# Optimization experiments

Measured on AMD Instinct MI355X. Metric: run time of the kernel, lower is better.

Reference implementation:

```python
import jax, jax.numpy as jnp
import numpy as np

N = 100000      # nodes
E = 1600000     # edges (avg degree 16)
DIN = 48        # input features
H = 48          # hidden
DOUT = 16       # output classes


def setup_inputs() -> dict:
    key = jax.random.key(0)
    ks = jax.random.split(key, 20)
    inp = {
        "x": jax.random.normal(ks[0], (N, DIN), jnp.float32),
        "edge_index": jax.random.randint(ks[1], (2, E), 0, N, jnp.int32),
    }
    # (name, in_dim, out_dim) for the 2-layer MLP in each of 3 GINConvs + final fc
    layers = [("11", DIN, H), ("12", H, H),
              ("21", H, H), ("22", H, H),
              ("31", H, H), ("32", H, H),
              ("f1", H, H), ("f2", H, DOUT)]
    for i, (nm, din, dout) in enumerate(layers):
        inp["w" + nm] = jax.random.normal(ks[2 + i], (din, dout), jnp.float32) / np.float32(np.sqrt(din))
        inp["b" + nm] = jax.random.normal(ks[10 + i], (dout,), jnp.float32) * 0.01
    return inp


def reference(x, edge_index, w11, b11, w12, b12, w21, b21, w22, b22,
              w31, b31, w32, b32, wf1, bf1, wf2, bf2):
    src, dst = edge_index[0], edge_index[1]
    n = x.shape[0]

    def gin_conv(h, w1, b1, w2, b2):
        # scatter-sum neighbor aggregation: sum_{j in N(i)} h_j
        agg = jax.ops.segment_sum(h[src], dst, num_segments=n)  # [N, d]
        h2 = h + agg  # eps = 0 (PyG GINConv default): (1+eps)*x + agg
        h2 = jax.nn.relu(h2 @ w1 + b1)
        return jax.nn.relu(h2 @ w2 + b2)

    h = gin_conv(x, w11, b11, w12, b12)
    h = gin_conv(h, w21, b21, w22, b22)
    h = gin_conv(h, w31, b31, w32, b32)
    # final fc head: Linear -> ReLU -> Linear
    return jax.nn.relu(h @ wf1 + bf1) @ wf2 + bf2
```

## Files before the change

### kernel.cpp

```cpp
#include <hip/hip_runtime.h>

#define NN 100000
#define NE 1600000
#define D 48
#define BK_SHIFT 8
#define BK_NODES 256
#define NBK 391
#define CAP 5120
#define EPB 4096
#define NBINB 391
#define ST 72

typedef _Float16 f16x8 __attribute__((ext_vector_type(8)));
typedef float f32x4 __attribute__((ext_vector_type(4)));


__global__ __launch_bounds__(256) void prepbin(
    const int* __restrict__ src, const int* __restrict__ dst,
    int* __restrict__ bucketLen, int* __restrict__ arena,
    const float* __restrict__ x,
    const float* __restrict__ w11, const float* __restrict__ w12,
    const float* __restrict__ w21, const float* __restrict__ w22,
    const float* __restrict__ w31, const float* __restrict__ w32,
    const float* __restrict__ wf1, const float* __restrict__ wf2,
    _Float16* __restrict__ wp, uint4* __restrict__ outh) {
    __shared__ int sCnt[NBK];
    __shared__ int sBase[NBK];
    int b = blockIdx.x;
    int tid = threadIdx.x;
    if (b < NBINB) {
        for (int i = tid; i < NBK; i += 256) sCnt[i] = 0;
        __syncthreads();
        int e0 = b * EPB;
        int eend = e0 + EPB;
        if (eend > NE) eend = NE;
        for (int i = e0 + tid; i < eend; i += 256) atomicAdd(&sCnt[dst[i] >> BK_SHIFT], 1);
        __syncthreads();
        for (int i = tid; i < NBK; i += 256) sBase[i] = atomicAdd(&bucketLen[i], sCnt[i]);
        __syncthreads();
        for (int i = tid; i < NBK; i += 256) sCnt[i] = 0;
        __syncthreads();
        for (int i = e0 + tid; i < eend; i += 256) {
            int d = dst[i];
            int bk = d >> BK_SHIFT;
            int off = atomicAdd(&sCnt[bk], 1) + sBase[bk];
            if (off < CAP) arena[bk * CAP + off] = ((d & (BK_NODES - 1)) << 17) | src[i];
        }
    } else if (b < NBINB + 8) {
        int l = b - NBINB;
        const float* W;
        int NL = 48;
        switch (l) {
            case 0: W = w11; break;
            case 1: W = w12; break;
            case 2: W = w21; break;
            case 3: W = w22; break;
            case 4: W = w31; break;
            case 5: W = w32; break;
            case 6: W = wf1; break;
            default: W = wf2; NL = 16; break;
        }
        _Float16* T = wp + l * 3072;
        int total = 64 * NL;
        for (int i = tid; i < total; i += 256) {
            int j = i & 7;
            int m = i >> 3;
            int g = m / NL;
            int nn = m - g * NL;
            int k = g * 8 + j;
            T[i] = (k < 48) ? (_Float16)W[k * NL + nn] : (_Float16)0.f;
        }
    } else {
        int i = (b - NBINB - 8) * 256 + tid;
        if (i < NN * 6) {
            const float4* p = (const float4*)(x + (size_t)i * 8);
            float4 a = p[0], bb = p[1];
            union { _Float16 h[8]; uint4 u; } pk;
            pk.h[0] = (_Float16)a.x; pk.h[1] = (_Float16)a.y;
            pk.h[2] = (_Float16)a.z; pk.h[3] = (_Float16)a.w;
            pk.h[4] = (_Float16)bb.x; pk.h[5] = (_Float16)bb.y;
            pk.h[6] = (_Float16)bb.z; pk.h[7] = (_Float16)bb.w;
            outh[i] = pk.u;
        }
    }
}


__global__ __launch_bounds__(256) void csr_from_bins(
    const int* __restrict__ arena, const int* __restrict__ bucketLen,
    int* __restrict__ rowptr, int* __restrict__ colidx) {
    __shared__ int sCnt[BK_NODES];
    __shared__ int sTot[256];
    int b = blockIdx.x;
    int tid = threadIdx.x;
    int len = bucketLen[b];
    if (len > CAP) len = CAP;
    const int* ar = arena + (size_t)b * CAP;
    int colBase = b * CAP;
    int nodeBase = b << BK_SHIFT;

    sCnt[tid] = 0;
    __syncthreads();
    for (int i = tid; i < len; i += 256) atomicAdd(&sCnt[ar[i] >> 17], 1);
    __syncthreads();

    int mine = sCnt[tid];
    sTot[tid] = mine;
    __syncthreads();
    for (int off = 1; off < 256; off <<= 1) {
        int add = 0;
        if (tid >= off) add = sTot[tid - off];
        __syncthreads();
        if (tid >= off) sTot[tid] += add;
        __syncthreads();
    }
    int excl = sTot[tid] - mine;
    int node = nodeBase + tid;
    if (node < NN) rowptr[node] = colBase + excl;
    __syncthreads();
    sCnt[tid] = colBase + excl;
    __syncthreads();
    for (int i = tid; i < len; i += 256) {
        int p = ar[i];
        int pos = atomicAdd(&sCnt[p >> 17], 1);
        colidx[pos] = p & 0x1FFFF;
    }
}


__device__ __forceinline__ void mfma_layer48(
    const _Float16* __restrict__ wp, const float* __restrict__ bias,
    const _Float16* src, _Float16* dst, int lane) {
    int am = lane & 15, q = lane >> 4;
    f16x8 a0 = *(const f16x8*)(src + am * ST + q * 8);
    f16x8 a1 = *(const f16x8*)(src + am * ST + 32 + q * 8);
#pragma unroll
    for (int t = 0; t < 3; ++t) {
        f16x8 b0 = *(const f16x8*)(wp + ((q) * 48 + t * 16 + am) * 8);
        f16x8 b1 = *(const f16x8*)(wp + ((4 + q) * 48 + t * 16 + am) * 8);
        float bv = bias[t * 16 + am];
        f32x4 c = {bv, bv, bv, bv};
        c = __builtin_amdgcn_mfma_f32_16x16x32_f16(a0, b0, c, 0, 0, 0);
        c = __builtin_amdgcn_mfma_f32_16x16x32_f16(a1, b1, c, 0, 0, 0);
#pragma unroll
        for (int r = 0; r < 4; ++r) {
            float v = fmaxf(c[r], 0.f);
            dst[(q * 4 + r) * ST + t * 16 + am] = (_Float16)v;
        }
    }
}


__device__ __forceinline__ void gather_stage(const uint4* __restrict__ hin4,
                                             const int* __restrict__ rowptr,
                                             const int* __restrict__ col,
                                             int bend,
                                             _Float16* s0, _Float16* s1,
                                             int base, int wv, int lane, int n) {
    for (int i = lane; i < 16 * 3; i += 64) {
        int r = i / 3, cq = i % 3;
        *(uint4*)(s0 + r * ST + 48 + cq * 8) = make_uint4(0u, 0u, 0u, 0u);
        *(uint4*)(s1 + r * ST + 48 + cq * 8) = make_uint4(0u, 0u, 0u, 0u);
    }
    int s = lane & 7;
    int c = lane >> 3;
    bool act = (c < 6);
    int cc = act ? c : 0;
    int nb = base + wv * 16;
    for (int nl = 0; nl < 16; nl += 2) {
        int node0 = nb + nl;
        int node1 = node0 + 1;
        f16x8 acc0 = {0, 0, 0, 0, 0, 0, 0, 0};
        f16x8 acc1 = {0, 0, 0, 0, 0, 0, 0, 0};
        int e00 = 0, e01 = 0, e10 = 0, e11 = 0;
        if (node0 < n) {
            e00 = rowptr[node0];
            e01 = rowptr[node0 + 1];
        }
        if (node1 < n) {
            e10 = e01;
            e11 = ((node1 & (BK_NODES - 1)) == BK_NODES - 1 || node1 == n - 1)
                      ? bend : rowptr[node1 + 1];
        }
        if (act) {
            int ebA = e00, ebB = e10;
            while (ebA < e01 || ebB < e11) {
                int eA0 = ebA + s, eA1 = ebA + 8 + s;
                int eB0 = ebB + s, eB1 = ebB + 8 + s;
                bool okA0 = eA0 < e01, okA1 = eA1 < e01;
                bool okB0 = eB0 < e11, okB1 = eB1 < e11;
                int iA0 = col[okA0 ? eA0 : e00] & 0x1FFFF;
                int iA1 = col[okA1 ? eA1 : e00] & 0x1FFFF;
                int iB0 = col[okB0 ? eB0 : e10] & 0x1FFFF;
                int iB1 = col[okB1 ? eB1 : e10] & 0x1FFFF;
                uint4 vA0 = hin4[(size_t)iA0 * 6 + cc];
                uint4 vA1 = hin4[(size_t)iA1 * 6 + cc];
                uint4 vB0 = hin4[(size_t)iB0 * 6 + cc];
                uint4 vB1 = hin4[(size_t)iB1 * 6 + cc];
                if (!okA0) vA0 = make_uint4(0u, 0u, 0u, 0u);
                if (!okA1) vA1 = make_uint4(0u, 0u, 0u, 0u);
                if (!okB0) vB0 = make_uint4(0u, 0u, 0u, 0u);
                if (!okB1) vB1 = make_uint4(0u, 0u, 0u, 0u);
                acc0 += *(const f16x8*)&vA0;
                acc0 += *(const f16x8*)&vA1;
                acc1 += *(const f16x8*)&vB0;
                acc1 += *(const f16x8*)&vB1;
                ebA += 16;
                ebB += 16;
            }
        }
        union { f16x8 f; int i[4]; } a0, a1, bx;
        a0.f = acc0;
        a1.f = acc1;
#pragma unroll
        for (int m = 1; m <= 4; m <<= 1) {
            bx.i[0] = __shfl_xor(a0.i[0], m);
            bx.i[1] = __shfl_xor(a0.i[1], m);
            bx.i[2] = __shfl_xor(a0.i[2], m);
            bx.i[3] = __shfl_xor(a0.i[3], m);
            a0.f += bx.f;
            bx.i[0] = __shfl_xor(a1.i[0], m);
            bx.i[1] = __shfl_xor(a1.i[1], m);
            bx.i[2] = __shfl_xor(a1.i[2], m);
            bx.i[3] = __shfl_xor(a1.i[3], m);
            a1.f += bx.f;
        }
        if (s == 0 && act) {
            union { f16x8 f; uint4 u; } r0, r1;
            r0.f = (f16x8){0, 0, 0, 0, 0, 0, 0, 0};
            r1.f = (f16x8){0, 0, 0, 0, 0, 0, 0, 0};
            if (node0 < n) {
                uint4 self = hin4[(size_t)node0 * 6 + c];
                r0.f = a0.f + *(const f16x8*)&self;
            }
            if (node1 < n) {
                uint4 self = hin4[(size_t)node1 * 6 + c];
                r1.f = a1.f + *(const f16x8*)&self;
            }
            *(uint4*)(s0 + nl * ST + c * 8) = r0.u;
            *(uint4*)(s0 + (nl + 1) * ST + c * 8) = r1.u;
        }
    }
    __builtin_amdgcn_wave_barrier();
}

__global__ __launch_bounds__(256) void conv_fused(
    const uint4* __restrict__ hin4, const int* __restrict__ rowptr,
    const int* __restrict__ col, const int* __restrict__ bucketLen,
    const _Float16* __restrict__ wp1, const float* __restrict__ B1,
    const _Float16* __restrict__ wp2, const float* __restrict__ B2,
    _Float16* __restrict__ hout, int n) {
    __shared__ __align__(16) _Float16 HA[2 * 64 * ST];
    int tid = threadIdx.x;
    int base = blockIdx.x * 64;
    int lane = tid & 63;
    int wv = tid >> 6;
    _Float16* s0 = HA + wv * 16 * ST;
    _Float16* s1 = HA + 64 * ST + wv * 16 * ST;

    int bucket = base >> BK_SHIFT;
    int blen = bucketLen[bucket];
    if (blen > CAP) blen = CAP;
    int bend = bucket * CAP + blen;

    gather_stage(hin4, rowptr, col, bend, s0, s1, base, wv, lane, n);
    mfma_layer48(wp1, B1, s0, s1, lane);
    __builtin_amdgcn_wave_barrier();

    int am = lane & 15, q = lane >> 4;
    f16x8 a0 = *(const f16x8*)(s1 + am * ST + q * 8);
    f16x8 a1 = *(const f16x8*)(s1 + am * ST + 32 + q * 8);
    int g0 = base + wv * 16;
#pragma unroll
    for (int t = 0; t < 3; ++t) {
        f16x8 b0 = *(const f16x8*)(wp2 + ((q) * 48 + t * 16 + am) * 8);
        f16x8 b1 = *(const f16x8*)(wp2 + ((4 + q) * 48 + t * 16 + am) * 8);
        float bv = B2[t * 16 + am];
        f32x4 c = {bv, bv, bv, bv};
        c = __builtin_amdgcn_mfma_f32_16x16x32_f16(a0, b0, c, 0, 0, 0);
        c = __builtin_amdgcn_mfma_f32_16x16x32_f16(a1, b1, c, 0, 0, 0);
#pragma unroll
        for (int r = 0; r < 4; ++r) {
            int node = g0 + q * 4 + r;
            if (node < n) {
                float v = fmaxf(c[r], 0.f);
                hout[(size_t)node * D + t * 16 + am] = (_Float16)v;
            }
        }
    }
}

__global__ __launch_bounds__(256) void tail_fused(
    const uint4* __restrict__ hin4, const int* __restrict__ rowptr,
    const int* __restrict__ col, const int* __restrict__ bucketLen,
    const _Float16* __restrict__ wp1, const float* __restrict__ B1,
    const _Float16* __restrict__ wp2, const float* __restrict__ B2,
    const _Float16* __restrict__ wp3, const float* __restrict__ B3,
    const _Float16* __restrict__ wp4, const float* __restrict__ B4,
    float* __restrict__ out, int n) {
    __shared__ __align__(16) _Float16 HA[2 * 64 * ST];
    int tid = threadIdx.x;
    int base = blockIdx.x * 64;
    int lane = tid & 63;
    int wv = tid >> 6;
    _Float16* s0 = HA + wv * 16 * ST;
    _Float16* s1 = HA + 64 * ST + wv * 16 * ST;

    int bucket = base >> BK_SHIFT;
    int blen = bucketLen[bucket];
    if (blen > CAP) blen = CAP;
    int bend = bucket * CAP + blen;

    gather_stage(hin4, rowptr, col, bend, s0, s1, base, wv, lane, n);
    mfma_layer48(wp1, B1, s0, s1, lane);
    __builtin_amdgcn_wave_barrier();
    mfma_layer48(wp2, B2, s1, s0, lane);
    __builtin_amdgcn_wave_barrier();
    mfma_layer48(wp3, B3, s0, s1, lane);
    __builtin_amdgcn_wave_barrier();

    int am = lane & 15, q = lane >> 4;
    f16x8 a0 = *(const f16x8*)(s1 + am * ST + q * 8);
    f16x8 a1 = *(const f16x8*)(s1 + am * ST + 32 + q * 8);
    f16x8 b0 = *(const f16x8*)(wp4 + ((q) * 16 + am) * 8);
    f16x8 b1 = *(const f16x8*)(wp4 + ((4 + q) * 16 + am) * 8);
    float bv = B4[am];
    f32x4 c = {bv, bv, bv, bv};
    c = __builtin_amdgcn_mfma_f32_16x16x32_f16(a0, b0, c, 0, 0, 0);
    c = __builtin_amdgcn_mfma_f32_16x16x32_f16(a1, b1, c, 0, 0, 0);
    int g0 = base + wv * 16;
#pragma unroll
    for (int r = 0; r < 4; ++r) {
        int node = g0 + q * 4 + r;
        if (node < n) out[(size_t)node * 16 + am] = c[r];
    }
}


extern "C" void kernel_launch(void* const* d_in, const int* in_sizes, int n_in,
                              void* d_out, int out_size, void* d_ws, size_t ws_size,
                              hipStream_t stream) {
    const int n = NN, e = NE;
    const float* x = (const float*)d_in[0];
    const int* ei = (const int*)d_in[1];
    const int* src = ei;
    const int* dst = ei + e;
    const float* w11 = (const float*)d_in[2];
    const float* b11 = (const float*)d_in[3];
    const float* w12 = (const float*)d_in[4];
    const float* b12 = (const float*)d_in[5];
    const float* w21 = (const float*)d_in[6];
    const float* b21 = (const float*)d_in[7];
    const float* w22 = (const float*)d_in[8];
    const float* b22 = (const float*)d_in[9];
    const float* w31 = (const float*)d_in[10];
    const float* b31 = (const float*)d_in[11];
    const float* w32 = (const float*)d_in[12];
    const float* b32 = (const float*)d_in[13];
    const float* wf1 = (const float*)d_in[14];
    const float* bf1 = (const float*)d_in[15];
    const float* wf2 = (const float*)d_in[16];
    const float* bf2 = (const float*)d_in[17];
    float* out = (float*)d_out;

    uint4* HAa = (uint4*)d_ws;
    uint4* HAb = HAa + (size_t)n * 6;
    _Float16* WP = (_Float16*)(HAb + (size_t)n * 6);
    int* rowptr = (int*)(WP + 8 * 3072);
    int* colidx = rowptr + (n + 1);
    int* arena = colidx + (size_t)NBK * CAP;
    int* bucketLen = arena + (size_t)NBK * CAP;
    size_t needed = (size_t)((char*)(bucketLen + NBK) - (char*)d_ws);
    if (needed > ws_size) return;

    const _Float16* wp11 = WP + 0 * 3072;
    const _Float16* wp12 = WP + 1 * 3072;
    const _Float16* wp21 = WP + 2 * 3072;
    const _Float16* wp22 = WP + 3 * 3072;
    const _Float16* wp31 = WP + 4 * 3072;
    const _Float16* wp32 = WP + 5 * 3072;
    const _Float16* wpf1 = WP + 6 * 3072;
    const _Float16* wpf2 = WP + 7 * 3072;

    hipMemsetAsync(bucketLen, 0, NBK * sizeof(int), stream);
    int gPB = NBINB + 8 + (n * 6 + 255) / 256;
    prepbin<<<gPB, 256, 0, stream>>>(src, dst, bucketLen, arena, x,
                                     w11, w12, w21, w22, w31, w32, wf1, wf2,
                                     WP, HAa);
    csr_from_bins<<<NBK, 256, 0, stream>>>(arena, bucketLen, rowptr, colidx);

    int gConv = (n + 63) / 64;

    conv_fused<<<gConv, 256, 0, stream>>>(HAa, rowptr, colidx, bucketLen,
                                          wp11, b11, wp12, b12, (_Float16*)HAb, n);
    conv_fused<<<gConv, 256, 0, stream>>>(HAb, rowptr, colidx, bucketLen,
                                          wp21, b21, wp22, b22, (_Float16*)HAa, n);
    tail_fused<<<gConv, 256, 0, stream>>>(HAa, rowptr, colidx, bucketLen,
                                          wp31, b31, wp32, b32,
                                          wpf1, bf1, wpf2, bf2, out, n);
}
```

Measured before the change: 273.5 us.

## Replace bucketed CSR build with fixed-capacity per-node adjacency slots

Drops the two-pass bucket binning and the csr_from_bins kernel. Each edge is now written directly into a fixed 64-slot row for its destination node using a global per-node atomic counter, and the gather reads those padded rows. This removes a kernel launch and the prefix-scan pass, at the cost of 1.6M global atomics on a 100K-entry counter array and a much larger padded arena. Any node with in-degree above 64 silently loses edges. Nontemporal loads and stores are also added for the column indices and the outputs.

```diff
diff --git a/kernel.cpp b/kernel.cpp
--- a/kernel.cpp
+++ b/kernel.cpp
@@ -3,12 +3,9 @@
 #define NN 100000
 #define NE 1600000
 #define D 48
-#define BK_SHIFT 8
-#define BK_NODES 256
-#define NBK 391
-#define CAP 5120
+#define CAPN 64
 #define EPB 4096
-#define NBINB 391
+#define NBB 391
 #define ST 72
 
 typedef _Float16 f16x8 __attribute__((ext_vector_type(8)));
@@ -17,37 +14,26 @@
 
 __global__ __launch_bounds__(256) void prepbin(
     const int* __restrict__ src, const int* __restrict__ dst,
-    int* __restrict__ bucketLen, int* __restrict__ arena,
+    int* __restrict__ cnt, int* __restrict__ arena,
     const float* __restrict__ x,
     const float* __restrict__ w11, const float* __restrict__ w12,
     const float* __restrict__ w21, const float* __restrict__ w22,
     const float* __restrict__ w31, const float* __restrict__ w32,
     const float* __restrict__ wf1, const float* __restrict__ wf2,
     _Float16* __restrict__ wp, uint4* __restrict__ outh) {
-    __shared__ int sCnt[NBK];
-    __shared__ int sBase[NBK];
     int b = blockIdx.x;
     int tid = threadIdx.x;
-    if (b < NBINB) {
-        for (int i = tid; i < NBK; i += 256) sCnt[i] = 0;
-        __syncthreads();
+    if (b < NBB) {
         int e0 = b * EPB;
         int eend = e0 + EPB;
         if (eend > NE) eend = NE;
-        for (int i = e0 + tid; i < eend; i += 256) atomicAdd(&sCnt[dst[i] >> BK_SHIFT], 1);
-        __syncthreads();
-        for (int i = tid; i < NBK; i += 256) sBase[i] = atomicAdd(&bucketLen[i], sCnt[i]);
-        __syncthreads();
-        for (int i = tid; i < NBK; i += 256) sCnt[i] = 0;
-        __syncthreads();
         for (int i = e0 + tid; i < eend; i += 256) {
             int d = dst[i];
-            int bk = d >> BK_SHIFT;
-            int off = atomicAdd(&sCnt[bk], 1) + sBase[bk];
-            if (off < CAP) arena[bk * CAP + off] = ((d & (BK_NODES - 1)) << 17) | src[i];
-        }
-    } else if (b < NBINB + 8) {
-        int l = b - NBINB;
+            int off = atomicAdd(&cnt[d], 1);
+            if (off < CAPN) arena[(size_t)d * CAPN + off] = src[i];
+        }
+    } else if (b < NBB + 8) {
+        int l = b - NBB;
         const float* W;
         int NL = 48;
         switch (l) {
@@ -71,7 +57,7 @@
             T[i] = (k < 48) ? (_Float16)W[k * NL + nn] : (_Float16)0.f;
         }
     } else {
-        int i = (b - NBINB - 8) * 256 + tid;
+        int i = (b - NBB - 8) * 256 + tid;
         if (i < NN * 6) {
             const float4* p = (const float4*)(x + (size_t)i * 8);
             float4 a = p[0], bb = p[1];
@@ -86,48 +72,6 @@
 }
 
 
-__global__ __launch_bounds__(256) void csr_from_bins(
-    const int* __restrict__ arena, const int* __restrict__ bucketLen,
-    int* __restrict__ rowptr, int* __restrict__ colidx) {
-    __shared__ int sCnt[BK_NODES];
-    __shared__ int sTot[256];
-    int b = blockIdx.x;
-    int tid = threadIdx.x;
-    int len = bucketLen[b];
-    if (len > CAP) len = CAP;
-    const int* ar = arena + (size_t)b * CAP;
-    int colBase = b * CAP;
-    int nodeBase = b << BK_SHIFT;
-
-    sCnt[tid] = 0;
-    __syncthreads();
-    for (int i = tid; i < len; i += 256) atomicAdd(&sCnt[ar[i] >> 17], 1);
-    __syncthreads();
-
-    int mine = sCnt[tid];
-    sTot[tid] = mine;
-    __syncthreads();
-    for (int off = 1; off < 256; off <<= 1) {
-        int add = 0;
-        if (tid >= off) add = sTot[tid - off];
-        __syncthreads();
-        if (tid >= off) sTot[tid] += add;
-        __syncthreads();
-    }
-    int excl = sTot[tid] - mine;
-    int node = nodeBase + tid;
-    if (node < NN) rowptr[node] = colBase + excl;
-    __syncthreads();
-    sCnt[tid] = colBase + excl;
-    __syncthreads();
-    for (int i = tid; i < len; i += 256) {
-        int p = ar[i];
-        int pos = atomicAdd(&sCnt[p >> 17], 1);
-        colidx[pos] = p & 0x1FFFF;
-    }
-}
-
-
 __device__ __forceinline__ void mfma_layer48(
     const _Float16* __restrict__ wp, const float* __restrict__ bias,
     const _Float16* src, _Float16* dst, int lane) {
@@ -152,9 +96,8 @@
 
 
 __device__ __forceinline__ void gather_stage(const uint4* __restrict__ hin4,
-                                             const int* __restrict__ rowptr,
+                                             const int* __restrict__ cnt,
                                              const int* __restrict__ col,
-                                             int bend,
                                              _Float16* s0, _Float16* s1,
                                              int base, int wv, int lane, int n) {
     for (int i = lane; i < 16 * 3; i += 64) {
@@ -170,29 +113,23 @@
     for (int nl = 0; nl < 16; nl += 2) {
         int node0 = nb + nl;
         int node1 = node0 + 1;
+        int len0 = 0, len1 = 0;
+        if (node0 < n) { len0 = cnt[node0]; if (len0 > CAPN) len0 = CAPN; }
+        if (node1 < n) { len1 = cnt[node1]; if (len1 > CAPN) len1 = CAPN; }
+        const int* colA = col + (size_t)(node0 < n ? node0 : 0) * CAPN;
+        const int* colB = col + (size_t)(node1 < n ? node1 : 0) * CAPN;
         f16x8 acc0 = {0, 0, 0, 0, 0, 0, 0, 0};
         f16x8 acc1 = {0, 0, 0, 0, 0, 0, 0, 0};
-        int e00 = 0, e01 = 0, e10 = 0, e11 = 0;
-        if (node0 < n) {
-            e00 = rowptr[node0];
-            e01 = rowptr[node0 + 1];
-        }
-        if (node1 < n) {
-            e10 = e01;
-            e11 = ((node1 & (BK_NODES - 1)) == BK_NODES - 1 || node1 == n - 1)
-                      ? bend : rowptr[node1 + 1];
-        }
+        int lmax = len0 > len1 ? len0 : len1;
         if (act) {
-            int ebA = e00, ebB = e10;
-            while (ebA < e01 || ebB < e11) {
-                int eA0 = ebA + s, eA1 = ebA + 8 + s;
-                int eB0 = ebB + s, eB1 = ebB + 8 + s;
-                bool okA0 = eA0 < e01, okA1 = eA1 < e01;
-                bool okB0 = eB0 < e11, okB1 = eB1 < e11;
-                int iA0 = col[okA0 ? eA0 : e00] & 0x1FFFF;
-                int iA1 = col[okA1 ? eA1 : e00] & 0x1FFFF;
-                int iB0 = col[okB0 ? eB0 : e10] & 0x1FFFF;
-                int iB1 = col[okB1 ? eB1 : e10] & 0x1FFFF;
+            for (int k = 0; k < lmax; k += 16) {
+                int k0 = k + s, k1 = k + 8 + s;
+                bool okA0 = k0 < len0, okA1 = k1 < len0;
+                bool okB0 = k0 < len1, okB1 = k1 < len1;
+                int iA0 = __builtin_nontemporal_load(colA + (okA0 ? k0 : 0)) & 0x1FFFF;
+                int iA1 = __builtin_nontemporal_load(colA + (okA1 ? k1 : 0)) & 0x1FFFF;
+                int iB0 = __builtin_nontemporal_load(colB + (okB0 ? k0 : 0)) & 0x1FFFF;
+                int iB1 = __builtin_nontemporal_load(colB + (okB1 ? k1 : 0)) & 0x1FFFF;
                 uint4 vA0 = hin4[(size_t)iA0 * 6 + cc];
                 uint4 vA1 = hin4[(size_t)iA1 * 6 + cc];
                 uint4 vB0 = hin4[(size_t)iB0 * 6 + cc];
@@ -205,8 +142,6 @@
                 acc0 += *(const f16x8*)&vA1;
                 acc1 += *(const f16x8*)&vB0;
                 acc1 += *(const f16x8*)&vB1;
-                ebA += 16;
-                ebB += 16;
             }
         }
         union { f16x8 f; int i[4]; } a0, a1, bx;
@@ -245,8 +180,8 @@
 }
 
 __global__ __launch_bounds__(256) void conv_fused(
-    const uint4* __restrict__ hin4, const int* __restrict__ rowptr,
-    const int* __restrict__ col, const int* __restrict__ bucketLen,
+    const uint4* __restrict__ hin4, const int* __restrict__ cnt,
+    const int* __restrict__ col,
     const _Float16* __restrict__ wp1, const float* __restrict__ B1,
     const _Float16* __restrict__ wp2, const float* __restrict__ B2,
     _Float16* __restrict__ hout, int n) {
@@ -258,12 +193,7 @@
     _Float16* s0 = HA + wv * 16 * ST;
     _Float16* s1 = HA + 64 * ST + wv * 16 * ST;
 
-    int bucket = base >> BK_SHIFT;
-    int blen = bucketLen[bucket];
-    if (blen > CAP) blen = CAP;
-    int bend = bucket * CAP + blen;
-
-    gather_stage(hin4, rowptr, col, bend, s0, s1, base, wv, lane, n);
+    gather_stage(hin4, cnt, col, s0, s1, base, wv, lane, n);
     mfma_layer48(wp1, B1, s0, s1, lane);
     __builtin_amdgcn_wave_barrier();
 
@@ -284,15 +214,16 @@
             int node = g0 + q * 4 + r;
             if (node < n) {
                 float v = fmaxf(c[r], 0.f);
-                hout[(size_t)node * D + t * 16 + am] = (_Float16)v;
+                __builtin_nontemporal_store((_Float16)v,
+                                            &hout[(size_t)node * D + t * 16 + am]);
             }
         }
     }
 }
 
 __global__ __launch_bounds__(256) void tail_fused(
-    const uint4* __restrict__ hin4, const int* __restrict__ rowptr,
-    const int* __restrict__ col, const int* __restrict__ bucketLen,
+    const uint4* __restrict__ hin4, const int* __restrict__ cnt,
+    const int* __restrict__ col,
     const _Float16* __restrict__ wp1, const float* __restrict__ B1,
     const _Float16* __restrict__ wp2, const float* __restrict__ B2,
     const _Float16* __restrict__ wp3, const float* __restrict__ B3,
@@ -306,12 +237,7 @@
     _Float16* s0 = HA + wv * 16 * ST;
     _Float16* s1 = HA + 64 * ST + wv * 16 * ST;
 
-    int bucket = base >> BK_SHIFT;
-    int blen = bucketLen[bucket];
-    if (blen > CAP) blen = CAP;
-    int bend = bucket * CAP + blen;
-
-    gather_stage(hin4, rowptr, col, bend, s0, s1, base, wv, lane, n);
+    gather_stage(hin4, cnt, col, s0, s1, base, wv, lane, n);
     mfma_layer48(wp1, B1, s0, s1, lane);
     __builtin_amdgcn_wave_barrier();
     mfma_layer48(wp2, B2, s1, s0, lane);
@@ -332,7 +258,7 @@
 #pragma unroll
     for (int r = 0; r < 4; ++r) {
         int node = g0 + q * 4 + r;
-        if (node < n) out[(size_t)node * 16 + am] = c[r];
+        if (node < n) __builtin_nontemporal_store(c[r], &out[(size_t)node * 16 + am]);
     }
 }
 
@@ -366,11 +292,9 @@
     uint4* HAa = (uint4*)d_ws;
     uint4* HAb = HAa + (size_t)n * 6;
     _Float16* WP = (_Float16*)(HAb + (size_t)n * 6);
-    int* rowptr = (int*)(WP + 8 * 3072);
-    int* colidx = rowptr + (n + 1);
-    int* arena = colidx + (size_t)NBK * CAP;
-    int* bucketLen = arena + (size_t)NBK * CAP;
-    size_t needed = (size_t)((char*)(bucketLen + NBK) - (char*)d_ws);
+    int* cnt = (int*)(WP + 8 * 3072);
+    int* arena = cnt + n;
+    size_t needed = (size_t)((char*)(arena + (size_t)n * CAPN) - (char*)d_ws);
     if (needed > ws_size) return;
 
     const _Float16* wp11 = WP + 0 * 3072;
@@ -382,20 +306,19 @@
     const _Float16* wpf1 = WP + 6 * 3072;
     const _Float16* wpf2 = WP + 7 * 3072;
 
-    hipMemsetAsync(bucketLen, 0, NBK * sizeof(int), stream);
-    int gPB = NBINB + 8 + (n * 6 + 255) / 256;
-    prepbin<<<gPB, 256, 0, stream>>>(src, dst, bucketLen, arena, x,
+    hipMemsetAsync(cnt, 0, (size_t)n * sizeof(int), stream);
+    int gPB = NBB + 8 + (n * 6 + 255) / 256;
+    prepbin<<<gPB, 256, 0, stream>>>(src, dst, cnt, arena, x,
                                      w11, w12, w21, w22, w31, w32, wf1, wf2,
                                      WP, HAa);
-    csr_from_bins<<<NBK, 256, 0, stream>>>(arena, bucketLen, rowptr, colidx);
 
     int gConv = (n + 63) / 64;
 
-    conv_fused<<<gConv, 256, 0, stream>>>(HAa, rowptr, colidx, bucketLen,
+    conv_fused<<<gConv, 256, 0, stream>>>(HAa, cnt, arena,
                                           wp11, b11, wp12, b12, (_Float16*)HAb, n);
-    conv_fused<<<gConv, 256, 0, stream>>>(HAb, rowptr, colidx, bucketLen,
+    conv_fused<<<gConv, 256, 0, stream>>>(HAb, cnt, arena,
                                           wp21, b21, wp22, b22, (_Float16*)HAa, n);
-    tail_fused<<<gConv, 256, 0, stream>>>(HAa, rowptr, colidx, bucketLen,
+    tail_fused<<<gConv, 256, 0, stream>>>(HAa, cnt, arena,
                                           wp31, b31, wp32, b32,
                                           wpf1, bf1, wpf2, bf2, out, n);
 }
```

New measurement: 368.4 us. 34.7% more time.

## Split CSR build into 64-node groups and rotate bucket atomic order

Applied to the files above, without the earlier changes.

The CSR construction kernel now runs one block per 64-node group (four groups per 256-node bin) instead of one block per bin. Each group block rescans its parent bin and keeps only its quarter, using a wave shuffle scan in place of a shared-memory scan with many barriers. Each group writes its own end offset for the conv kernels to use. The binning kernel also rotates the order of its global bucket atomics per block and skips zero counts, to reduce contention on the same counters. The trade-off is that every bin slice is read four times, and the per-group capacity adds a new truncation point if a group has too many edges.

```diff
diff --git a/kernel.cpp b/kernel.cpp
--- a/kernel.cpp
+++ b/kernel.cpp
@@ -9,6 +9,8 @@
 #define CAP 5120
 #define EPB 4096
 #define NBINB 391
+#define NG 1563
+#define CAPG 1344
 #define ST 72
 
 typedef _Float16 f16x8 __attribute__((ext_vector_type(8)));
@@ -36,7 +38,13 @@
         if (eend > NE) eend = NE;
         for (int i = e0 + tid; i < eend; i += 256) atomicAdd(&sCnt[dst[i] >> BK_SHIFT], 1);
         __syncthreads();
-        for (int i = tid; i < NBK; i += 256) sBase[i] = atomicAdd(&bucketLen[i], sCnt[i]);
+        int rot = (b * 101) % NBK;
+        for (int k = tid; k < NBK; k += 256) {
+            int i = k + rot;
+            if (i >= NBK) i -= NBK;
+            int v = sCnt[i];
+            sBase[i] = v ? atomicAdd(&bucketLen[i], v) : 0;
+        }
         __syncthreads();
         for (int i = tid; i < NBK; i += 256) sCnt[i] = 0;
         __syncthreads();
@@ -44,7 +52,7 @@
             int d = dst[i];
             int bk = d >> BK_SHIFT;
             int off = atomicAdd(&sCnt[bk], 1) + sBase[bk];
-            if (off < CAP) arena[bk * CAP + off] = ((d & (BK_NODES - 1)) << 17) | src[i];
+            if (off < CAP) arena[(size_t)bk * CAP + off] = ((d & (BK_NODES - 1)) << 17) | src[i];
         }
     } else if (b < NBINB + 8) {
         int l = b - NBINB;
@@ -86,44 +94,53 @@
 }
 
 
-__global__ __launch_bounds__(256) void csr_from_bins(
+__global__ __launch_bounds__(256) void csr64(
     const int* __restrict__ arena, const int* __restrict__ bucketLen,
-    int* __restrict__ rowptr, int* __restrict__ colidx) {
-    __shared__ int sCnt[BK_NODES];
-    __shared__ int sTot[256];
-    int b = blockIdx.x;
+    int* __restrict__ rowptr, int* __restrict__ gEnd, int* __restrict__ colidx) {
+    __shared__ int sCnt[64];
+    __shared__ int sPos[64];
+    int g = blockIdx.x;
     int tid = threadIdx.x;
-    int len = bucketLen[b];
-    if (len > CAP) len = CAP;
-    const int* ar = arena + (size_t)b * CAP;
-    int colBase = b * CAP;
-    int nodeBase = b << BK_SHIFT;
-
-    sCnt[tid] = 0;
+    int parent = g >> 2;
+    int quarter = g & 3;
+    int plen = bucketLen[parent];
+    if (plen > CAP) plen = CAP;
+    const int* slice = arena + (size_t)parent * CAP;
+    int gBase = g * CAPG;
+
+    if (tid < 64) sCnt[tid] = 0;
     __syncthreads();
-    for (int i = tid; i < len; i += 256) atomicAdd(&sCnt[ar[i] >> 17], 1);
+    for (int i = tid; i < plen; i += 256) {
+        int p = slice[i];
+        if ((p >> 23) == quarter) atomicAdd(&sCnt[(p >> 17) & 63], 1);
+    }
     __syncthreads();
-
-    int mine = sCnt[tid];
-    sTot[tid] = mine;
+    if (tid < 64) {
+        int v = sCnt[tid];
+        int xx = v;
+#pragma unroll
+        for (int off = 1; off < 64; off <<= 1) {
+            int y = __shfl_up(xx, off);
+            if (tid >= off) xx += y;
+        }
+        int excl = xx - v;
+        if (excl > CAPG) excl = CAPG;
+        int node = (g << 6) + tid;
+        if (node < NN) rowptr[node] = gBase + excl;
+        sPos[tid] = gBase + excl;
+        if (tid == 63) {
+            int tot = xx > CAPG ? CAPG : xx;
+            gEnd[g] = gBase + tot;
+        }
+    }
     __syncthreads();
-    for (int off = 1; off < 256; off <<= 1) {
-        int add = 0;
-        if (tid >= off) add = sTot[tid - off];
-        __syncthreads();
-        if (tid >= off) sTot[tid] += add;
-        __syncthreads();
-    }
-    int excl = sTot[tid] - mine;
-    int node = nodeBase + tid;
-    if (node < NN) rowptr[node] = colBase + excl;
-    __syncthreads();
-    sCnt[tid] = colBase + excl;
-    __syncthreads();
-    for (int i = tid; i < len; i += 256) {
-        int p = ar[i];
-        int pos = atomicAdd(&sCnt[p >> 17], 1);
-        colidx[pos] = p & 0x1FFFF;
+    int lim = gBase + CAPG;
+    for (int i = tid; i < plen; i += 256) {
+        int p = slice[i];
+        if ((p >> 23) == quarter) {
+            int slot = atomicAdd(&sPos[(p >> 17) & 63], 1);
+            if (slot < lim) colidx[slot] = p & 0x1FFFF;
+        }
     }
 }
 
@@ -154,7 +171,7 @@
 __device__ __forceinline__ void gather_stage(const uint4* __restrict__ hin4,
                                              const int* __restrict__ rowptr,
                                              const int* __restrict__ col,
-                                             int bend,
+                                             int gend,
                                              _Float16* s0, _Float16* s1,
                                              int base, int wv, int lane, int n) {
     for (int i = lane; i < 16 * 3; i += 64) {
@@ -170,6 +187,7 @@
     for (int nl = 0; nl < 16; nl += 2) {
         int node0 = nb + nl;
         int node1 = node0 + 1;
+        int r1 = wv * 16 + nl + 1;
         f16x8 acc0 = {0, 0, 0, 0, 0, 0, 0, 0};
         f16x8 acc1 = {0, 0, 0, 0, 0, 0, 0, 0};
         int e00 = 0, e01 = 0, e10 = 0, e11 = 0;
@@ -179,8 +197,7 @@
         }
         if (node1 < n) {
             e10 = e01;
-            e11 = ((node1 & (BK_NODES - 1)) == BK_NODES - 1 || node1 == n - 1)
-                      ? bend : rowptr[node1 + 1];
+            e11 = (r1 == 63 || node1 == n - 1) ? gend : rowptr[node1 + 1];
         }
         if (act) {
             int ebA = e00, ebB = e10;
@@ -226,19 +243,19 @@
             a1.f += bx.f;
         }
         if (s == 0 && act) {
-            union { f16x8 f; uint4 u; } r0, r1;
-            r0.f = (f16x8){0, 0, 0, 0, 0, 0, 0, 0};
-            r1.f = (f16x8){0, 0, 0, 0, 0, 0, 0, 0};
+            union { f16x8 f; uint4 u; } r0u, r1u;
+            r0u.f = (f16x8){0, 0, 0, 0, 0, 0, 0, 0};
+            r1u.f = (f16x8){0, 0, 0, 0, 0, 0, 0, 0};
             if (node0 < n) {
                 uint4 self = hin4[(size_t)node0 * 6 + c];
-                r0.f = a0.f + *(const f16x8*)&self;
+                r0u.f = a0.f + *(const f16x8*)&self;
             }
             if (node1 < n) {
                 uint4 self = hin4[(size_t)node1 * 6 + c];
-                r1.f = a1.f + *(const f16x8*)&self;
+                r1u.f = a1.f + *(const f16x8*)&self;
             }
-            *(uint4*)(s0 + nl * ST + c * 8) = r0.u;
-            *(uint4*)(s0 + (nl + 1) * ST + c * 8) = r1.u;
+            *(uint4*)(s0 + nl * ST + c * 8) = r0u.u;
+            *(uint4*)(s0 + (nl + 1) * ST + c * 8) = r1u.u;
         }
     }
     __builtin_amdgcn_wave_barrier();
@@ -246,24 +263,22 @@
 
 __global__ __launch_bounds__(256) void conv_fused(
     const uint4* __restrict__ hin4, const int* __restrict__ rowptr,
-    const int* __restrict__ col, const int* __restrict__ bucketLen,
+    const int* __restrict__ col, const int* __restrict__ gEnd,
     const _Float16* __restrict__ wp1, const float* __restrict__ B1,
     const _Float16* __restrict__ wp2, const float* __restrict__ B2,
     _Float16* __restrict__ hout, int n) {
     __shared__ __align__(16) _Float16 HA[2 * 64 * ST];
     int tid = threadIdx.x;
-    int base = blockIdx.x * 64;
+    int g = blockIdx.x;
+    int base = g << 6;
     int lane = tid & 63;
     int wv = tid >> 6;
     _Float16* s0 = HA + wv * 16 * ST;
     _Float16* s1 = HA + 64 * ST + wv * 16 * ST;
 
-    int bucket = base >> BK_SHIFT;
-    int blen = bucketLen[bucket];
-    if (blen > CAP) blen = CAP;
-    int bend = bucket * CAP + blen;
-
-    gather_stage(hin4, rowptr, col, bend, s0, s1, base, wv, lane, n);
+    int gend = gEnd[g];
+
+    gather_stage(hin4, rowptr, col, gend, s0, s1, base, wv, lane, n);
     mfma_layer48(wp1, B1, s0, s1, lane);
     __builtin_amdgcn_wave_barrier();
 
@@ -292,7 +307,7 @@
 
 __global__ __launch_bounds__(256) void tail_fused(
     const uint4* __restrict__ hin4, const int* __restrict__ rowptr,
-    const int* __restrict__ col, const int* __restrict__ bucketLen,
+    const int* __restrict__ col, const int* __restrict__ gEnd,
     const _Float16* __restrict__ wp1, const float* __restrict__ B1,
     const _Float16* __restrict__ wp2, const float* __restrict__ B2,
     const _Float16* __restrict__ wp3, const float* __restrict__ B3,
@@ -300,18 +315,16 @@
     float* __restrict__ out, int n) {
     __shared__ __align__(16) _Float16 HA[2 * 64 * ST];
     int tid = threadIdx.x;
-    int base = blockIdx.x * 64;
+    int g = blockIdx.x;
+    int base = g << 6;
     int lane = tid & 63;
     int wv = tid >> 6;
     _Float16* s0 = HA + wv * 16 * ST;
     _Float16* s1 = HA + 64 * ST + wv * 16 * ST;
 
-    int bucket = base >> BK_SHIFT;
-    int blen = bucketLen[bucket];
-    if (blen > CAP) blen = CAP;
-    int bend = bucket * CAP + blen;
-
-    gather_stage(hin4, rowptr, col, bend, s0, s1, base, wv, lane, n);
+    int gend = gEnd[g];
+
+    gather_stage(hin4, rowptr, col, gend, s0, s1, base, wv, lane, n);
     mfma_layer48(wp1, B1, s0, s1, lane);
     __builtin_amdgcn_wave_barrier();
     mfma_layer48(wp2, B2, s1, s0, lane);
@@ -367,8 +380,9 @@
     uint4* HAb = HAa + (size_t)n * 6;
     _Float16* WP = (_Float16*)(HAb + (size_t)n * 6);
     int* rowptr = (int*)(WP + 8 * 3072);
-    int* colidx = rowptr + (n + 1);
-    int* arena = colidx + (size_t)NBK * CAP;
+    int* gEnd = rowptr + n;
+    int* colidx = gEnd + NG;
+    int* arena = colidx + (size_t)NG * CAPG;
     int* bucketLen = arena + (size_t)NBK * CAP;
     size_t needed = (size_t)((char*)(bucketLen + NBK) - (char*)d_ws);
     if (needed > ws_size) return;
@@ -387,15 +401,15 @@
     prepbin<<<gPB, 256, 0, stream>>>(src, dst, bucketLen, arena, x,
                                      w11, w12, w21, w22, w31, w32, wf1, wf2,
                                      WP, HAa);
-    csr_from_bins<<<NBK, 256, 0, stream>>>(arena, bucketLen, rowptr, colidx);
-
-    int gConv = (n + 63) / 64;
-
-    conv_fused<<<gConv, 256, 0, stream>>>(HAa, rowptr, colidx, bucketLen,
+    csr64<<<NG, 256, 0, stream>>>(arena, bucketLen, rowptr, gEnd, colidx);
+
+    int gConv = NG;
+
+    conv_fused<<<gConv, 256, 0, stream>>>(HAa, rowptr, colidx, gEnd,
                                           wp11, b11, wp12, b12, (_Float16*)HAb, n);
-    conv_fused<<<gConv, 256, 0, stream>>>(HAb, rowptr, colidx, bucketLen,
+    conv_fused<<<gConv, 256, 0, stream>>>(HAb, rowptr, colidx, gEnd,
                                           wp21, b21, wp22, b22, (_Float16*)HAa, n);
-    tail_fused<<<gConv, 256, 0, stream>>>(HAa, rowptr, colidx, bucketLen,
+    tail_fused<<<gConv, 256, 0, stream>>>(HAa, rowptr, colidx, gEnd,
                                           wp31, b31, wp32, b32,
                                           wpf1, bf1, wpf2, bf2, out, n);
 }
```

Result: no change. 271.4 us (-0.8%).
